# Kernel tuning notes

Measured on AMD Instinct MI355X. Metric: run time of the kernel, lower is better.

Reference implementation:

```python
import jax, jax.numpy as jnp
import numpy as np

BS, S, E, H = 64, 512, 1024, 16
HD = E // H
MASK_ID, KNOW_ID = 30001, 30002


def setup_inputs() -> dict:
    key = jax.random.key(0)
    ks = jax.random.split(key, 8)
    model_output = jax.random.normal(ks[0], (BS, S, E), dtype=jnp.float32)
    ids = jax.random.randint(ks[1], (BS, S), 0, 30000)  # never hits special ids
    ids = ids.at[:, 0].set(MASK_ID)        # exactly one [MASK] per sequence
    ids = ids.at[:, 1:9].set(KNOW_ID)      # 8 knowledge slots per sequence
    knowledge_output = jax.random.normal(ks[2], (BS, E), dtype=jnp.float32)
    empty_knowledge_mask = jax.random.randint(ks[3], (BS,), 0, 2).astype(bool)
    bound = 1.0 / np.sqrt(E)
    in_proj_weight = jax.random.uniform(ks[4], (3 * E, E), minval=-bound, maxval=bound, dtype=jnp.float32)
    in_proj_bias = jnp.zeros((3 * E,), jnp.float32)
    out_proj_weight = jax.random.uniform(ks[5], (E, E), minval=-bound, maxval=bound, dtype=jnp.float32)
    out_proj_bias = jnp.zeros((E,), jnp.float32)
    attention_strength = jnp.float32(0.1)
    return {
        "model_output": model_output,
        "knowledge_output": knowledge_output,
        "in_proj_weight": in_proj_weight,
        "in_proj_bias": in_proj_bias,
        "out_proj_weight": out_proj_weight,
        "out_proj_bias": out_proj_bias,
        "attention_strength": attention_strength,
        "input_ids": ids,
        "empty_knowledge_mask": empty_knowledge_mask,
        "knowledge_token_id": KNOW_ID,
        "mask_token_id": MASK_ID,
    }


def reference(model_output, knowledge_output, in_proj_weight, in_proj_bias,
              out_proj_weight, out_proj_bias, attention_strength,
              input_ids, empty_knowledge_mask, knowledge_token_id, mask_token_id):
    bs, sent_len, hidden = model_output.shape
    # --- knowledge injection: scatter knowledge vector into knowledge-token slots ---
    knowledge_mask = input_ids == knowledge_token_id                 # [bs, S]
    kv_src = jnp.where(knowledge_mask[:, :, None],
                       knowledge_output[:, None, :], model_output)  # [bs, S, E]
    # --- single-query gather: one [MASK] position per sequence ---
    mask_pos = jnp.argmax(input_ids == mask_token_id, axis=1)        # [bs]
    q_in = jnp.take_along_axis(kv_src, mask_pos[:, None, None], axis=1)[:, 0, :]  # [bs, E]
    # --- nn.MultiheadAttention (eval mode, dropout=0) ---
    Wq, Wk, Wv = in_proj_weight[:E], in_proj_weight[E:2 * E], in_proj_weight[2 * E:]
    bq, bk, bv = in_proj_bias[:E], in_proj_bias[E:2 * E], in_proj_bias[2 * E:]
    q = (q_in @ Wq.T + bq).reshape(bs, H, HD)                        # [bs, H, hd]
    k = (kv_src @ Wk.T + bk).reshape(bs, sent_len, H, HD)            # [bs, S, H, hd]
    v = (kv_src @ Wv.T + bv).reshape(bs, sent_len, H, HD)
    scale = 1.0 / np.sqrt(HD)
    scores = jnp.einsum('bhd,bshd->bhs', q * scale, k)               # [bs, H, S]
    attn = jax.nn.softmax(scores, axis=-1)
    ctx = jnp.einsum('bhs,bshd->bhd', attn, v).reshape(bs, hidden)   # [bs, E]
    attn_output = ctx @ out_proj_weight.T + out_proj_bias            # [bs, E]
    # --- residual on the ORIGINAL (pre-injection) mask-token states ---
    origin_q = jnp.take_along_axis(model_output, mask_pos[:, None, None], axis=1)[:, 0, :]
    mask_output = origin_q + attention_strength * attn_output
    # --- conditional restore where knowledge is empty ---
    mask_output = jnp.where(empty_knowledge_mask[:, None], origin_q, mask_output)
    return mask_output
```

## Files before the change

kernel.cpp:

```cpp
#include <hip/hip_runtime.h>

#define BS 64
#define S  512
#define E  1024
#define H  16
#define HD 64
#define SCALE 0.125f
#define CATT 8

#define W_QIN  1024
#define W_QKBF 66560
#define W_NUM  1115136
#define W_DEN  9503744
#define W_CTX  9511936

typedef __attribute__((ext_vector_type(8))) short short8;
typedef __attribute__((ext_vector_type(4))) float floatx4;

union S8u { uint2 u2[2]; short8 s; };

__device__ __forceinline__ unsigned short bf16c(float x) {
    unsigned int u = __float_as_uint(x);
    return (unsigned short)((u + 0x7fffu + ((u >> 16) & 1u)) >> 16);
}
__device__ __forceinline__ unsigned int pack_bf16(float a, float b) {
    return (unsigned int)bf16c(a) | ((unsigned int)bf16c(b) << 16);
}
__device__ __forceinline__ void fma4(float4& acc, float s, const float4& v) {
    acc.x += s * v.x; acc.y += s * v.y; acc.z += s * v.z; acc.w += s * v.w;
}
__device__ __forceinline__ float dot4(const float4& a, const float4& b) {
    return a.x * b.x + a.y * b.y + a.z * b.z + a.w * b.w;
}
__device__ __forceinline__ void bfly8(float* a) {
    #pragma unroll
    for (int off = 32; off > 0; off >>= 1) {
        #pragma unroll
        for (int i = 0; i < 8; i++) a[i] += __shfl_xor(a[i], off, 64);
    }
}

__global__ void k_prep(const float* __restrict__ model, const float* __restrict__ knowledge,
                       const int* __restrict__ ids, const int* __restrict__ mask_id_p,
                       const int* __restrict__ kid_p, int* __restrict__ mp,
                       float* __restrict__ qin) {
    int b = blockIdx.x, tid = threadIdx.x;
    __shared__ int best;
    if (tid == 0) best = S;
    __syncthreads();
    int mid = mask_id_p[0];
    for (int s = tid; s < S; s += 256)
        if (ids[b * S + s] == mid) atomicMin(&best, s);
    __syncthreads();
    int m = (best == S) ? 0 : best;
    if (tid == 0) mp[b] = m;
    bool isk = (ids[b * S + m] == kid_p[0]);
    const float* qrow = isk ? knowledge + (size_t)b * E : model + ((size_t)(b * S + m)) * E;
    ((float4*)(qin + (size_t)b * E))[tid] = ((const float4*)qrow)[tid];
}

__global__ void k_qgen(const float* __restrict__ qin, const float* __restrict__ w_in,
                       const float* __restrict__ b_in, unsigned short* __restrict__ qkbf) {
    int h = blockIdx.x, b0 = blockIdx.y * 4, t = threadIdx.x;
    __shared__ float qin_l[4][1024];
    __shared__ float qred[4][64][4];
    __shared__ float qs_l[4][64];
    #pragma unroll
    for (int k = 0; k < 4; k++) {
        int idx4 = k * 256 + t;
        int bb = idx4 >> 8, col = (idx4 & 255) * 4;
        *(float4*)&qin_l[bb][col] = *(const float4*)(qin + (size_t)(b0 + bb) * E + col);
    }
    __syncthreads();
    {
        int d = t >> 2, part = t & 3;
        const float* wr = w_in + (size_t)(h * HD + d) * E + part * 256;
        float acc[4] = {0.f, 0.f, 0.f, 0.f};
        for (int i = 0; i < 64; i++) {
            float4 wv = *(const float4*)(wr + i * 4);
            #pragma unroll
            for (int bb = 0; bb < 4; bb++)
                acc[bb] += dot4(wv, *(const float4*)&qin_l[bb][part * 256 + i * 4]);
        }
        #pragma unroll
        for (int bb = 0; bb < 4; bb++) qred[bb][d][part] = acc[bb];
    }
    __syncthreads();
    if (t < 64) {
        float bias = b_in[h * HD + t];
        #pragma unroll
        for (int bb = 0; bb < 4; bb++)
            qs_l[bb][t] = qred[bb][t][0] + qred[bb][t][1] + qred[bb][t][2] + qred[bb][t][3] + bias;
    }
    __syncthreads();
    {
        int e0 = t * 4;
        const float* wk = w_in + (size_t)(E + h * HD) * E + e0;
        float4 acc[4];
        #pragma unroll
        for (int bb = 0; bb < 4; bb++) acc[bb] = make_float4(0.f, 0.f, 0.f, 0.f);
        for (int d = 0; d < HD; d++) {
            float4 wv = *(const float4*)(wk + (size_t)d * E);
            #pragma unroll
            for (int bb = 0; bb < 4; bb++) fma4(acc[bb], qs_l[bb][d], wv);
        }
        #pragma unroll
        for (int bb = 0; bb < 4; bb++) {
            uint2 pk;
            pk.x = pack_bf16(acc[bb].x * SCALE, acc[bb].y * SCALE);
            pk.y = pack_bf16(acc[bb].z * SCALE, acc[bb].w * SCALE);
            *(uint2*)&qkbf[((size_t)(b0 + bb) * H + h) * E + e0] = pk;
        }
    }
}

__global__ __launch_bounds__(512, 4) void k_attn(
    const float* __restrict__ model, const float* __restrict__ knowledge,
    const int* __restrict__ ids, const int* __restrict__ kid_p,
    const unsigned short* __restrict__ qkbf, float* __restrict__ num, float* __restrict__ den) {
    __shared__ __align__(16) unsigned char Ubuf[73984];
    unsigned short* Rbuf  = (unsigned short*)Ubuf;
    unsigned short* RbufT = (unsigned short*)(Ubuf + 33024);
    float* Tbuf = (float*)Ubuf;
    __shared__ unsigned short Pbuf[16 * 40];
    __shared__ float Sred[4][16][17];
    __shared__ unsigned long long kmask_s;

    int tid = threadIdx.x;
    int w = tid >> 6, l = tid & 63;
    int quad = l >> 4, lm = l & 15;
    int c = blockIdx.x, b = blockIdx.y;
    int s0 = c * 64;

    if (w == 0) {
        int id = ids[b * S + s0 + l];
        unsigned long long mk = __ballot(id == kid_p[0]);
        if (l == 0) kmask_s = mk;
    }
    floatx4 accn[8];
    #pragma unroll
    for (int i = 0; i < 8; i++) accn[i] = (floatx4)0.f;
    float accden = 0.f;
    const float* kb = knowledge + (size_t)b * E;
    const float* mb = model + (size_t)b * S * E;
    const unsigned short* qh = qkbf + ((size_t)b * H + lm) * E;
    __syncthreads();
    unsigned long long kmask = kmask_s;

    for (int pass = 0; pass < 4; pass++) {
        int rb = pass * 16;
        #pragma unroll
        for (int g = 0; g < 4; g++) {
            int r0 = g * 4;
            const float* rp0 = ((kmask >> (rb + r0 + 0)) & 1ull) ? kb : mb + (size_t)(s0 + rb + r0 + 0) * E;
            const float* rp1 = ((kmask >> (rb + r0 + 1)) & 1ull) ? kb : mb + (size_t)(s0 + rb + r0 + 1) * E;
            const float* rp2 = ((kmask >> (rb + r0 + 2)) & 1ull) ? kb : mb + (size_t)(s0 + rb + r0 + 2) * E;
            const float* rp3 = ((kmask >> (rb + r0 + 3)) & 1ull) ? kb : mb + (size_t)(s0 + rb + r0 + 3) * E;
            #pragma unroll
            for (int cc = 0; cc < 2; cc++) {
                int col = cc * 512 + tid;
                unsigned short h0 = bf16c(rp0[col]);
                unsigned short h1 = bf16c(rp1[col]);
                unsigned short h2 = bf16c(rp2[col]);
                unsigned short h3 = bf16c(rp3[col]);
                Rbuf[(r0 + 0) * 1032 + col] = h0;
                Rbuf[(r0 + 1) * 1032 + col] = h1;
                Rbuf[(r0 + 2) * 1032 + col] = h2;
                Rbuf[(r0 + 3) * 1032 + col] = h3;
                uint2 pk;
                pk.x = (unsigned int)h0 | ((unsigned int)h1 << 16);
                pk.y = (unsigned int)h2 | ((unsigned int)h3 << 16);
                *(uint2*)&RbufT[col * 20 + r0] = pk;
            }
        }
        __syncthreads();
        if (w < 4) {
            floatx4 acs = (floatx4)0.f;
            #pragma unroll
            for (int t = 0; t < 8; t++) {
                int kk = w * 8 + t;
                short8 a  = *(const short8*)(const void*)&Rbuf[lm * 1032 + kk * 32 + quad * 8];
                short8 bf = *(const short8*)(const void*)(qh + kk * 32 + quad * 8);
                acs = __builtin_amdgcn_mfma_f32_16x16x32_bf16(a, bf, acs, 0, 0, 0);
            }
            Sred[w][quad * 4 + 0][lm] = acs[0];
            Sred[w][quad * 4 + 1][lm] = acs[1];
            Sred[w][quad * 4 + 2][lm] = acs[2];
            Sred[w][quad * 4 + 3][lm] = acs[3];
        }
        __syncthreads();
        if (w == 0) {
            float ex[4];
            #pragma unroll
            for (int r = 0; r < 4; r++) {
                int row = quad * 4 + r;
                float s = Sred[0][row][lm] + Sred[1][row][lm] + Sred[2][row][lm] + Sred[3][row][lm];
                ex[r] = __expf(s);
                accden += ex[r];
            }
            uint2 pw;
            pw.x = (unsigned int)bf16c(ex[0]) | ((unsigned int)bf16c(ex[1]) << 16);
            pw.y = (unsigned int)bf16c(ex[2]) | ((unsigned int)bf16c(ex[3]) << 16);
            *(uint2*)&Pbuf[lm * 40 + quad * 4] = pw;
        }
        __syncthreads();
        short8 afr = {};
        if (quad < 2) afr = *(const short8*)(const void*)&Pbuf[lm * 40 + quad * 8];
        #pragma unroll
        for (int i = 0; i < 8; i++) {
            int e = (w * 8 + i) * 16 + lm;
            S8u bb; bb.s = (short8){};
            if (quad < 2) {
                bb.u2[0] = *(const uint2*)&RbufT[e * 20 + quad * 8];
                bb.u2[1] = *(const uint2*)&RbufT[e * 20 + quad * 8 + 4];
            }
            accn[i] = __builtin_amdgcn_mfma_f32_16x16x32_bf16(afr, bb.s, accn[i], 0, 0, 0);
        }
        __syncthreads();
    }
    #pragma unroll
    for (int i = 0; i < 8; i++) {
        int e = (w * 8 + i) * 16 + lm;
        Tbuf[(quad * 4 + 0) * 1028 + e] = accn[i][0];
        Tbuf[(quad * 4 + 1) * 1028 + e] = accn[i][1];
        Tbuf[(quad * 4 + 2) * 1028 + e] = accn[i][2];
        Tbuf[(quad * 4 + 3) * 1028 + e] = accn[i][3];
    }
    if (w == 0) {
        accden += __shfl_xor(accden, 16, 64);
        accden += __shfl_xor(accden, 32, 64);
        if (l < 16) den[(size_t)(c * BS + b) * H + l] = accden;
    }
    __syncthreads();
    size_t base = ((size_t)(c * BS + b) * H) * E;
    #pragma unroll
    for (int k = 0; k < 8; k++) {
        int idx4 = k * 512 + tid;
        int h = idx4 >> 8, e4 = (idx4 & 255) * 4;
        *(float4*)(num + base + (size_t)idx4 * 4) = *(const float4*)&Tbuf[h * 1028 + e4];
    }
}

__global__ void k_pc(const float* __restrict__ num, const float* __restrict__ den,
                     const float* __restrict__ w_in, const float* __restrict__ b_in,
                     float* __restrict__ ctx) {
    int h = blockIdx.x, b0 = blockIdx.y * 4, t = threadIdx.x;
    __shared__ float p_l[4][1024];
    __shared__ float cred[4][64][4];
    __shared__ float inv_l[4];
    #pragma unroll
    for (int k = 0; k < 4; k++) {
        int idx4 = k * 256 + t;
        int bb = idx4 >> 8, e4 = (idx4 & 255) * 4;
        float4 a = make_float4(0.f, 0.f, 0.f, 0.f);
        for (int cc = 0; cc < CATT; cc++) {
            float4 v = *(const float4*)(num + (((size_t)(cc * BS + b0 + bb) * H + h) * E) + e4);
            a.x += v.x; a.y += v.y; a.z += v.z; a.w += v.w;
        }
        *(float4*)&p_l[bb][e4] = a;
    }
    if (t < 4) {
        float ds = 0.f;
        for (int cc = 0; cc < CATT; cc++) ds += den[(size_t)(cc * BS + b0 + t) * H + h];
        inv_l[t] = 1.0f / ds;
    }
    __syncthreads();
    {
        int jj = t >> 2, part = t & 3;
        const float* wr = w_in + (size_t)(2 * E + h * HD + jj) * E + part * 256;
        float acc[4] = {0.f, 0.f, 0.f, 0.f};
        for (int i = 0; i < 64; i++) {
            float4 wv = *(const float4*)(wr + i * 4);
            #pragma unroll
            for (int bb = 0; bb < 4; bb++)
                acc[bb] += dot4(wv, *(const float4*)&p_l[bb][part * 256 + i * 4]);
        }
        #pragma unroll
        for (int bb = 0; bb < 4; bb++) cred[bb][jj][part] = acc[bb];
    }
    __syncthreads();
    if (t < 64) {
        float bias = b_in[2 * E + h * HD + t];
        #pragma unroll
        for (int bb = 0; bb < 4; bb++) {
            float s = cred[bb][t][0] + cred[bb][t][1] + cred[bb][t][2] + cred[bb][t][3];
            ctx[(size_t)(b0 + bb) * E + h * HD + t] = inv_l[bb] * s + bias;
        }
    }
}

__global__ void k_out(const float* __restrict__ model, const float* __restrict__ w_out,
                      const float* __restrict__ b_out, const float* __restrict__ ctx,
                      const int* __restrict__ mp, const int* __restrict__ empty,
                      const float* __restrict__ strength_p, float* __restrict__ out) {
    int w = threadIdx.x >> 6, l = threadIdx.x & 63;
    int j = blockIdx.x * 4 + w;
    int b0 = blockIdx.y * 8;
    const float* wr = w_out + (size_t)j * E;
    float4 wv[4];
    #pragma unroll
    for (int r = 0; r < 4; r++) wv[r] = *(const float4*)(wr + r * 256 + l * 4);
    float acc[8];
    #pragma unroll
    for (int bb = 0; bb < 8; bb++) {
        const float* src = ctx + (size_t)(b0 + bb) * E;
        float a = 0.f;
        #pragma unroll
        for (int r = 0; r < 4; r++) a += dot4(wv[r], *(const float4*)(src + r * 256 + l * 4));
        acc[bb] = a;
    }
    bfly8(acc);
    if (l < 8) {
        float myacc = acc[0];
        #pragma unroll
        for (int bb = 1; bb < 8; bb++) myacc = (l == bb) ? acc[bb] : myacc;
        int b = b0 + l;
        int m = mp[b];
        float orig = model[((size_t)(b * S + m)) * E + j];
        float bias = b_out[j];
        float st = strength_p[0];
        out[(size_t)b * E + j] = empty[b] ? orig : orig + st * (myacc + bias);
    }
}

extern "C" void kernel_launch(void* const* d_in, const int* in_sizes, int n_in,
                              void* d_out, int out_size, void* d_ws, size_t ws_size,
                              hipStream_t stream) {
    const float* model     = (const float*)d_in[0];
    const float* knowledge = (const float*)d_in[1];
    const float* w_in      = (const float*)d_in[2];
    const float* b_in      = (const float*)d_in[3];
    const float* w_out     = (const float*)d_in[4];
    const float* b_out     = (const float*)d_in[5];
    const float* strength  = (const float*)d_in[6];
    const int*   ids       = (const int*)d_in[7];
    const int*   empty     = (const int*)d_in[8];
    const int*   know_id   = (const int*)d_in[9];
    const int*   mask_id   = (const int*)d_in[10];
    float* out = (float*)d_out;

    float* ws  = (float*)d_ws;
    int*   mp  = (int*)d_ws;
    float* qin = ws + W_QIN;
    unsigned short* qkbf = (unsigned short*)(ws + W_QKBF);
    float* num = ws + W_NUM;
    float* den = ws + W_DEN;
    float* ctx = ws + W_CTX;

    k_prep<<<BS, 256, 0, stream>>>(model, knowledge, ids, mask_id, know_id, mp, qin);
    k_qgen<<<dim3(H, 16), 256, 0, stream>>>(qin, w_in, b_in, qkbf);
    k_attn<<<dim3(CATT, BS), 512, 0, stream>>>(model, knowledge, ids, know_id, qkbf, num, den);
    k_pc<<<dim3(H, 16), 256, 0, stream>>>(num, den, w_in, b_in, ctx);
    k_out<<<dim3(256, 8), 256, 0, stream>>>(model, w_out, b_out, ctx, mp, empty, strength, out);
}
```

Measured before the change: 280.9 us.

## Prefetch next K/V rows into registers and hoist query fragments in attention kernel

The attention kernel now loads each 16-row chunk as float4 into registers, then writes it to shared memory as bf16. It issues the global loads for the next pass right after the barrier, so the fetch overlaps the MFMA score and context work. Query fragments are loaded into registers once instead of being re-read from global memory on every pass. The grid is transposed so that consecutive blocks take different batches, and several inner loops get unroll pragmas. In exchange, register pressure rises and the transposed-buffer stores become scalar 16-bit writes, which may cause LDS bank conflicts.

New measurement: 292.7 us. +4.2%, slower.

```diff
diff --git a/kernel.cpp b/kernel.cpp
--- a/kernel.cpp
+++ b/kernel.cpp
@@ -76,6 +76,7 @@
         int d = t >> 2, part = t & 3;
         const float* wr = w_in + (size_t)(h * HD + d) * E + part * 256;
         float acc[4] = {0.f, 0.f, 0.f, 0.f};
+        #pragma unroll 8
         for (int i = 0; i < 64; i++) {
             float4 wv = *(const float4*)(wr + i * 4);
             #pragma unroll
@@ -99,6 +100,7 @@
         float4 acc[4];
         #pragma unroll
         for (int bb = 0; bb < 4; bb++) acc[bb] = make_float4(0.f, 0.f, 0.f, 0.f);
+        #pragma unroll 8
         for (int d = 0; d < HD; d++) {
             float4 wv = *(const float4*)(wk + (size_t)d * E);
             #pragma unroll
@@ -129,7 +131,7 @@
     int tid = threadIdx.x;
     int w = tid >> 6, l = tid & 63;
     int quad = l >> 4, lm = l & 15;
-    int c = blockIdx.x, b = blockIdx.y;
+    int b = blockIdx.x, c = blockIdx.y;
     int s0 = c * 64;
 
     if (w == 0) {
@@ -143,45 +145,61 @@
     float accden = 0.f;
     const float* kb = knowledge + (size_t)b * E;
     const float* mb = model + (size_t)b * S * E;
-    const unsigned short* qh = qkbf + ((size_t)b * H + lm) * E;
+    short8 qfr[8];
+    if (w < 4) {
+        const unsigned short* qh = qkbf + ((size_t)b * H + lm) * E;
+        #pragma unroll
+        for (int t = 0; t < 8; t++)
+            qfr[t] = *(const short8*)(const void*)(qh + (w * 8 + t) * 32 + quad * 8);
+    }
     __syncthreads();
     unsigned long long kmask = kmask_s;
 
+    int hi = tid >> 8;
+    int col4 = (tid & 255) * 4;
+    const float* base0 = mb + (size_t)(s0 + hi) * E + col4;
+    const float* kbase = kb + col4;
+
+    float4 pf[8];
+    #pragma unroll
+    for (int k = 0; k < 8; k++) {
+        int s = k * 2 + hi;
+        const float* rp = ((kmask >> s) & 1ull) ? kbase : base0 + (size_t)(k * 2) * E;
+        pf[k] = *(const float4*)rp;
+    }
+
     for (int pass = 0; pass < 4; pass++) {
-        int rb = pass * 16;
-        #pragma unroll
-        for (int g = 0; g < 4; g++) {
-            int r0 = g * 4;
-            const float* rp0 = ((kmask >> (rb + r0 + 0)) & 1ull) ? kb : mb + (size_t)(s0 + rb + r0 + 0) * E;
-            const float* rp1 = ((kmask >> (rb + r0 + 1)) & 1ull) ? kb : mb + (size_t)(s0 + rb + r0 + 1) * E;
-            const float* rp2 = ((kmask >> (rb + r0 + 2)) & 1ull) ? kb : mb + (size_t)(s0 + rb + r0 + 2) * E;
-            const float* rp3 = ((kmask >> (rb + r0 + 3)) & 1ull) ? kb : mb + (size_t)(s0 + rb + r0 + 3) * E;
-            #pragma unroll
-            for (int cc = 0; cc < 2; cc++) {
-                int col = cc * 512 + tid;
-                unsigned short h0 = bf16c(rp0[col]);
-                unsigned short h1 = bf16c(rp1[col]);
-                unsigned short h2 = bf16c(rp2[col]);
-                unsigned short h3 = bf16c(rp3[col]);
-                Rbuf[(r0 + 0) * 1032 + col] = h0;
-                Rbuf[(r0 + 1) * 1032 + col] = h1;
-                Rbuf[(r0 + 2) * 1032 + col] = h2;
-                Rbuf[(r0 + 3) * 1032 + col] = h3;
-                uint2 pk;
-                pk.x = (unsigned int)h0 | ((unsigned int)h1 << 16);
-                pk.y = (unsigned int)h2 | ((unsigned int)h3 << 16);
-                *(uint2*)&RbufT[col * 20 + r0] = pk;
+        #pragma unroll
+        for (int k = 0; k < 8; k++) {
+            int row = k * 2 + hi;
+            float4 v = pf[k];
+            unsigned short h0 = bf16c(v.x), h1 = bf16c(v.y), h2 = bf16c(v.z), h3 = bf16c(v.w);
+            uint2 pk;
+            pk.x = (unsigned int)h0 | ((unsigned int)h1 << 16);
+            pk.y = (unsigned int)h2 | ((unsigned int)h3 << 16);
+            *(uint2*)&Rbuf[row * 1032 + col4] = pk;
+            RbufT[(col4 + 0) * 20 + row] = h0;
+            RbufT[(col4 + 1) * 20 + row] = h1;
+            RbufT[(col4 + 2) * 20 + row] = h2;
+            RbufT[(col4 + 3) * 20 + row] = h3;
+        }
+        __syncthreads();
+        if (pass < 3) {
+            int rb = (pass + 1) * 16;
+            #pragma unroll
+            for (int k = 0; k < 8; k++) {
+                int s = rb + k * 2 + hi;
+                const float* rp = ((kmask >> s) & 1ull) ? kbase : base0 + (size_t)(rb + k * 2) * E;
+                pf[k] = *(const float4*)rp;
             }
         }
-        __syncthreads();
         if (w < 4) {
             floatx4 acs = (floatx4)0.f;
             #pragma unroll
             for (int t = 0; t < 8; t++) {
                 int kk = w * 8 + t;
-                short8 a  = *(const short8*)(const void*)&Rbuf[lm * 1032 + kk * 32 + quad * 8];
-                short8 bf = *(const short8*)(const void*)(qh + kk * 32 + quad * 8);
-                acs = __builtin_amdgcn_mfma_f32_16x16x32_bf16(a, bf, acs, 0, 0, 0);
+                short8 a = *(const short8*)(const void*)&Rbuf[lm * 1032 + kk * 32 + quad * 8];
+                acs = __builtin_amdgcn_mfma_f32_16x16x32_bf16(a, qfr[t], acs, 0, 0, 0);
             }
             Sred[w][quad * 4 + 0][lm] = acs[0];
             Sred[w][quad * 4 + 1][lm] = acs[1];
@@ -253,6 +271,7 @@
         int idx4 = k * 256 + t;
         int bb = idx4 >> 8, e4 = (idx4 & 255) * 4;
         float4 a = make_float4(0.f, 0.f, 0.f, 0.f);
+        #pragma unroll
         for (int cc = 0; cc < CATT; cc++) {
             float4 v = *(const float4*)(num + (((size_t)(cc * BS + b0 + bb) * H + h) * E) + e4);
             a.x += v.x; a.y += v.y; a.z += v.z; a.w += v.w;
@@ -269,6 +288,7 @@
         int jj = t >> 2, part = t & 3;
         const float* wr = w_in + (size_t)(2 * E + h * HD + jj) * E + part * 256;
         float acc[4] = {0.f, 0.f, 0.f, 0.f};
+        #pragma unroll 8
         for (int i = 0; i < 64; i++) {
             float4 wv = *(const float4*)(wr + i * 4);
             #pragma unroll
@@ -349,7 +369,7 @@
 
     k_prep<<<BS, 256, 0, stream>>>(model, knowledge, ids, mask_id, know_id, mp, qin);
     k_qgen<<<dim3(H, 16), 256, 0, stream>>>(qin, w_in, b_in, qkbf);
-    k_attn<<<dim3(CATT, BS), 512, 0, stream>>>(model, knowledge, ids, know_id, qkbf, num, den);
+    k_attn<<<dim3(BS, CATT), 512, 0, stream>>>(model, knowledge, ids, know_id, qkbf, num, den);
     k_pc<<<dim3(H, 16), 256, 0, stream>>>(num, den, w_in, b_in, ctx);
     k_out<<<dim3(256, 8), 256, 0, stream>>>(model, w_out, b_out, ctx, mp, empty, strength, out);
 }
```
